# Optimization experiments

Measured on AMD Instinct MI355X. Metric: run time of the kernel, lower is better.

The kernel has to match this reference:

```python
import jax, jax.numpy as jnp
import numpy as np

B, NQ, NK, D, H = 2, 2048, 4096, 1024, 16
HD = D // H
SCALE = HD ** -0.5
NEG = -1e20


def setup_inputs() -> dict:
    key = jax.random.key(0)
    ks = jax.random.split(key, 9)
    w_std = D ** -0.5
    return {
        "q": jax.random.normal(ks[0], (B, NQ, D), dtype=jnp.float32),
        "k": jax.random.normal(ks[1], (B, NK, D), dtype=jnp.float32),
        "v": jax.random.normal(ks[2], (B, NK, D), dtype=jnp.float32),
        "key_padding_mask": jax.random.bernoulli(ks[3], 0.1, (B, NK)),
        "Wq": jax.random.normal(ks[4], (D, D), dtype=jnp.float32) * w_std,
        "Wk": jax.random.normal(ks[5], (D, D), dtype=jnp.float32) * w_std,
        "Wv": jax.random.normal(ks[6], (D, D), dtype=jnp.float32) * w_std,
        "Wp": jax.random.normal(ks[7], (D, D), dtype=jnp.float32) * w_std,
        "bp": jax.random.normal(ks[8], (D,), dtype=jnp.float32) * 0.01,
    }


def reference(q, k, v, key_padding_mask, Wq, Wk, Wv, Wp, bp):
    # linear projections (no bias, qkv_bias=False)
    qh = (q @ Wq.T).reshape(B, NQ, H, HD).transpose(0, 2, 1, 3)  # [B,H,NQ,HD]
    kh = (k @ Wk.T).reshape(B, NK, H, HD).transpose(0, 2, 1, 3)  # [B,H,NK,HD]
    vh = (v @ Wv.T).reshape(B, NK, H, HD).transpose(0, 2, 1, 3)  # [B,H,NK,HD]
    scores = jnp.einsum("bhqd,bhkd->bhqk", qh, kh)               # [B,H,NQ,NK]
    # mask BEFORE scaling (faithful to original order), then scale + softmax
    scores = jnp.where(key_padding_mask[:, None, None, :], NEG, scores)
    attn = jax.nn.softmax(scores * SCALE, axis=-1)
    out = jnp.einsum("bhqk,bhkd->bhqd", attn, vh)                # [B,H,NQ,HD]
    out = out.transpose(0, 2, 1, 3).reshape(B, NQ, D)
    x = out @ Wp.T + bp
    return x
```

## Files before the change

### kernel.cpp

```cpp
#include <hip/hip_runtime.h>


typedef __attribute__((ext_vector_type(8))) short bf16x8;
typedef __attribute__((ext_vector_type(4))) short bf16x4;
typedef __attribute__((ext_vector_type(4))) float f32x4;
typedef __attribute__((ext_vector_type(4))) unsigned short u16x4;
typedef unsigned short u16;
typedef unsigned char u8;

#define DEV __device__ __forceinline__

DEV u16 f2bf(float f) {
  union { float f; unsigned int u; } x; x.f = f;
  unsigned int u = x.u;
  return (u16)((u + 0x7fffu + ((u >> 16) & 1u)) >> 16);
}

DEV unsigned cvt_pk_bf16(float lo, float hi) {
  unsigned r;
  asm("v_cvt_pk_bf16_f32 %0, %1, %2" : "=v"(r) : "v"(lo), "v"(hi));
  return r;
}

DEV u16x4 cvt4_bf16(float4 v) {
  union { unsigned u[2]; u16x4 s; } uu;
  uu.u[0] = cvt_pk_bf16(v.x, v.y);
  uu.u[1] = cvt_pk_bf16(v.z, v.w);
  return uu.s;
}

DEV void gload16(const void* g, void* l) {
  __builtin_amdgcn_global_load_lds(
      (const __attribute__((address_space(1))) void*)g,
      (__attribute__((address_space(3))) void*)l, 16, 0, 0);
}

#define MASK_BIAS (-1.8033688e19f)
#define FREE_BIAS (-16.0f)
#define SCALE_LOG2E 0.18033688f

__global__ void prep_k(
    const float* __restrict__ Wq, const float* __restrict__ Wk,
    const float* __restrict__ Wv, const float* __restrict__ Wp,
    const float* __restrict__ q, const float* __restrict__ k, const float* __restrict__ v,
    u16* __restrict__ wqb, u16* __restrict__ wkb, u16* __restrict__ wvb, u16* __restrict__ wpb,
    u16* __restrict__ qb, u16* __restrict__ kb, u16* __restrict__ vb, int total,
    const u8* __restrict__ raw, float* __restrict__ biasf)
{
  if (blockIdx.x == gridDim.x - 1) {
    int t = threadIdx.x;
    int f_off = 0, f_gt1 = 0, f_80 = 0;
    for (int i = t; i < 8192; i += 256) {
      u8 bv = raw[i];
      if (bv > 1) f_gt1 = 1;
      if ((i & 3) && bv) f_off = 1;
      if (((i & 3) == 0) && bv == 0x80) f_80 = 1;
    }
    int g_gt1 = __syncthreads_or(f_gt1);
    int g_off = __syncthreads_or(f_off);
    int g_80  = __syncthreads_or(f_80);
    for (int i = t; i < 8192; i += 256) {
      int vv;
      if (g_gt1) {
        if (g_80) vv = (((const u16*)raw)[i] != 0) ? 1 : 0;
        else      vv = (((const float*)raw)[i] != 0.0f) ? 1 : 0;
      } else if (g_off) {
        vv = raw[i] ? 1 : 0;
      } else {
        vv = (((const int*)raw)[i] != 0) ? 1 : 0;
      }
      biasf[i] = vv ? MASK_BIAS : FREE_BIAS;
    }
    return;
  }
  int stride = (gridDim.x - 1) * blockDim.x;
  for (int idx = blockIdx.x * blockDim.x + threadIdx.x; idx < total; idx += stride) {
    const float* src; u16* dst; int off;
    if (idx < 131072)       { src = Wq; dst = wqb; off = idx; }
    else if (idx < 262144)  { src = Wk; dst = wkb; off = idx - 131072; }
    else if (idx < 393216)  { src = Wv; dst = wvb; off = idx - 262144; }
    else if (idx < 524288)  { src = Wp; dst = wpb; off = idx - 393216; }
    else if (idx < 1048576) { src = q;  dst = qb;  off = idx - 524288; }
    else if (idx < 2097152) { src = k;  dst = kb;  off = idx - 1048576; }
    else                    { src = v;  dst = vb;  off = idx - 2097152; }
    float4 a = *reinterpret_cast<const float4*>(src + (size_t)off * 8);
    float4 bq = *reinterpret_cast<const float4*>(src + (size_t)off * 8 + 4);
    union { unsigned u[4]; uint4 q4; } o;
    o.u[0] = cvt_pk_bf16(a.x, a.y); o.u[1] = cvt_pk_bf16(a.z, a.w);
    o.u[2] = cvt_pk_bf16(bq.x, bq.y); o.u[3] = cvt_pk_bf16(bq.z, bq.w);
    *reinterpret_cast<uint4*>(dst + (size_t)off * 8) = o.q4;
  }
}

template <bool ABF>
__global__ __launch_bounds__(256) void proj_fused(
    const float* __restrict__ qf32, const float* __restrict__ kf32, const float* __restrict__ vf32,
    const u16* __restrict__ qb, const u16* __restrict__ kb, const u16* __restrict__ vb,
    const u16* __restrict__ wqb, const u16* __restrict__ wkb, const u16* __restrict__ wvb,
    u16* __restrict__ qh, u16* __restrict__ kh, u16* __restrict__ vh)
{
  constexpr int K = 1024;
  __shared__ __align__(16) u16 As[128 * 32];
  __shared__ __align__(16) u16 Bs[128 * 32];
  const int tid = threadIdx.x;
  const int lane = tid & 63;
  const int w = tid >> 6;
  const int wm = w >> 1, wn = w & 1;
  const int l15 = lane & 15, lg = lane >> 4;

  int bid = blockIdx.x;
  bid = (bid & 7) * 160 + (bid >> 3);
  int seg, local;
  if (bid < 256)      { seg = 0; local = bid; }
  else if (bid < 768) { seg = 1; local = bid - 256; }
  else                { seg = 2; local = bid - 768; }
  const int bm = local >> 3, bn = local & 7;
  const float* Af = seg == 0 ? qf32 : (seg == 1 ? kf32 : vf32);
  const u16* Ab   = seg == 0 ? qb   : (seg == 1 ? kb   : vb);
  const u16* Wb   = seg == 0 ? wqb  : (seg == 1 ? wkb  : wvb);
  u16* outh       = seg == 0 ? qh   : (seg == 1 ? kh   : vh);
  const int sl = (seg == 0) ? 11 : 12;

  f32x4 acc[4][4] = {};

  for (int k0 = 0; k0 < K; k0 += 32) {
    __syncthreads();
    if constexpr (ABF) {
#pragma unroll
      for (int i = 0; i < 2; ++i) {
        int f = tid + 256 * i;
        int row = f >> 2, c = f & 3;
        gload16(Ab + (size_t)(bm * 128 + row) * K + k0 + c * 8, (char*)As + f * 16);
        gload16(Wb + (size_t)(bn * 128 + row) * K + k0 + c * 8, (char*)Bs + f * 16);
      }
    } else {
#pragma unroll
      for (int i = 0; i < 2; ++i) {
        int f = tid + 256 * i;
        int row = f >> 2, c = f & 3;
        gload16(Wb + (size_t)(bn * 128 + row) * K + k0 + c * 8, (char*)Bs + f * 16);
      }
#pragma unroll
      for (int i = 0; i < 4; ++i) {
        int f = tid + 256 * i;
        int row = f >> 3, c4 = f & 7;
        float4 va = *reinterpret_cast<const float4*>(Af + (size_t)(bm * 128 + row) * K + k0 + c4 * 4);
        *reinterpret_cast<u16x4*>((char*)As + row * 64 + c4 * 8) = cvt4_bf16(va);
      }
    }
    __syncthreads();

    bf16x8 af[4], bfr[4];
#pragma unroll
    for (int mi = 0; mi < 4; ++mi)
      af[mi] = *reinterpret_cast<const bf16x8*>((const char*)As + (wm * 64 + mi * 16 + l15) * 64 + lg * 16);
#pragma unroll
    for (int ni = 0; ni < 4; ++ni)
      bfr[ni] = *reinterpret_cast<const bf16x8*>((const char*)Bs + (wn * 64 + ni * 16 + l15) * 64 + lg * 16);
#pragma unroll
    for (int mi = 0; mi < 4; ++mi)
#pragma unroll
      for (int ni = 0; ni < 4; ++ni)
        acc[mi][ni] = __builtin_amdgcn_mfma_f32_16x16x32_bf16(af[mi], bfr[ni], acc[mi][ni], 0, 0, 0);
  }

  const int seqmask = (1 << sl) - 1;
#pragma unroll
  for (int mi = 0; mi < 4; ++mi)
#pragma unroll
    for (int ni = 0; ni < 4; ++ni)
#pragma unroll
      for (int r = 0; r < 4; ++r) {
        int m = bm * 128 + wm * 64 + mi * 16 + lg * 4 + r;
        int n = bn * 128 + wn * 64 + ni * 16 + l15;
        int b = m >> sl, ml = m & seqmask;
        int h = n >> 6, hd = n & 63;
        outh[((((size_t)b * 16 + h) << sl) + ml) * 64 + hd] = f2bf(acc[mi][ni][r]);
      }
}

__global__ __launch_bounds__(512, 2) void attn_k(
    const u16* __restrict__ qh, const u16* __restrict__ kh, const u16* __restrict__ vh,
    const float* __restrict__ biasf, u16* __restrict__ ao)
{
  __shared__ __align__(16) u16 lds[17920];

  const int tid = threadIdx.x;
  const int lane = tid & 63;
  const int w = tid >> 6;
  const int l15 = lane & 15, lg = lane >> 4;

  int bid = blockIdx.x;
  bid = (bid & 7) * 32 + (bid >> 3);
  const int qt = bid & 7;
  const int bh = bid >> 3;
  const int b = bh >> 4, h = bh & 15;

  const size_t base_kv = (size_t)bh * 4096 * 64;

  bf16x8 qf0[2], qf1[2];
  {
    const u16* qp0 = qh + ((size_t)bh * 2048 + (size_t)qt * 256 + w * 16 + l15) * 64 + lg * 8;
    qf0[0] = *reinterpret_cast<const bf16x8*>(qp0);
    qf0[1] = *reinterpret_cast<const bf16x8*>(qp0 + 32);
    const u16* qp1 = qp0 + 128 * 64;
    qf1[0] = *reinterpret_cast<const bf16x8*>(qp1);
    qf1[1] = *reinterpret_cast<const bf16x8*>(qp1 + 32);
  }

  f32x4 o0[4] = {}, o1[4] = {};
  float lac0 = 0.f, lac1 = 0.f;
  const float* bpt = biasf + b * 4096 + lg * 4;

  const int kp = tid >> 3, c8v = tid & 7;
  const u16* kg = kh + base_kv + (size_t)tid * 8;
  const u16* vg = vh + base_kv + (size_t)(2 * kp) * 64 + c8v * 8;
  const int kcol = (tid & 7) * 8;
  const int krow0 = tid >> 3, krow1 = krow0 + 32;
  int vst[8];
#pragma unroll
  for (int j = 0; j < 8; ++j) {
    int d = c8v * 8 + j;
    vst[j] = (d * 136 + kp * 4) ^ (((d >> 3) & 7) << 3);
  }
  int vrd[4][4];
#pragma unroll
  for (int dt = 0; dt < 4; ++dt)
#pragma unroll
    for (int n = 0; n < 4; ++n) {
      int d = dt * 16 + l15;
      vrd[dt][n] = ((d * 136 + (n * 16 + lg * 4) * 2)) ^ (((d >> 3) & 7) << 3);
    }

  uint4 kr0, kr1, vr0, vr1;
  if (w < 4) {
    kr0 = *reinterpret_cast<const uint4*>(kg);
    kr1 = *reinterpret_cast<const uint4*>(kg + 2048);
    vr0 = *reinterpret_cast<const uint4*>(vg);
    vr1 = *reinterpret_cast<const uint4*>(vg + 64);
    u16 (*K0)[72] = reinterpret_cast<u16(*)[72]>(lds);
    u16* V0 = lds + 4608;
    *reinterpret_cast<uint4*>(&K0[krow0][kcol]) = kr0;
    *reinterpret_cast<uint4*>(&K0[krow1][kcol]) = kr1;
    const u16* pa = reinterpret_cast<const u16*>(&vr0);
    const u16* pb = reinterpret_cast<const u16*>(&vr1);
#pragma unroll
    for (int j = 0; j < 8; ++j) {
      ushort2 t2; t2.x = pa[j]; t2.y = pb[j];
      *reinterpret_cast<ushort2*>(reinterpret_cast<char*>(V0) + vst[j]) = t2;
    }
    kg += 4096; vg += 4096;
    kr0 = *reinterpret_cast<const uint4*>(kg);
    kr1 = *reinterpret_cast<const uint4*>(kg + 2048);
    vr0 = *reinterpret_cast<const uint4*>(vg);
    vr1 = *reinterpret_cast<const uint4*>(vg + 64);
  }
  __syncthreads();

  for (int t = 0; t < 64; ++t) {
    u16* bufc = lds + (t & 1) * 8960;
    u16 (*Ks)[72] = reinterpret_cast<u16(*)[72]>(bufc);
    u16* Vt = bufc + 4608;

    if (w < 4 && t < 63) {
      u16* bufn = lds + ((t & 1) ^ 1) * 8960;
      u16 (*Kn)[72] = reinterpret_cast<u16(*)[72]>(bufn);
      u16* Vn = bufn + 4608;
      *reinterpret_cast<uint4*>(&Kn[krow0][kcol]) = kr0;
      *reinterpret_cast<uint4*>(&Kn[krow1][kcol]) = kr1;
      const u16* pa = reinterpret_cast<const u16*>(&vr0);
      const u16* pb = reinterpret_cast<const u16*>(&vr1);
#pragma unroll
      for (int j = 0; j < 8; ++j) {
        ushort2 t2; t2.x = pa[j]; t2.y = pb[j];
        *reinterpret_cast<ushort2*>(reinterpret_cast<char*>(Vn) + vst[j]) = t2;
      }
      if (t < 62) {
        kg += 4096; vg += 4096;
        kr0 = *reinterpret_cast<const uint4*>(kg);
        kr1 = *reinterpret_cast<const uint4*>(kg + 2048);
        vr0 = *reinterpret_cast<const uint4*>(vg);
        vr1 = *reinterpret_cast<const uint4*>(vg + 64);
      }
    }

    float4 bA[4];
#pragma unroll
    for (int n = 0; n < 4; ++n)
      bA[n] = *reinterpret_cast<const float4*>(bpt + n * 16);

    f32x4 s0[4], s1[4];
    __builtin_amdgcn_s_setprio(1);
#pragma unroll
    for (int n = 0; n < 4; ++n) {
      bf16x8 k0f = *reinterpret_cast<const bf16x8*>(&Ks[n * 16 + l15][lg * 8]);
      bf16x8 k1f = *reinterpret_cast<const bf16x8*>(&Ks[n * 16 + l15][32 + lg * 8]);
      f32x4 z0 = {};
      z0 = __builtin_amdgcn_mfma_f32_16x16x32_bf16(k0f, qf0[0], z0, 0, 0, 0);
      z0 = __builtin_amdgcn_mfma_f32_16x16x32_bf16(k1f, qf0[1], z0, 0, 0, 0);
      s0[n] = z0;
      f32x4 z1 = {};
      z1 = __builtin_amdgcn_mfma_f32_16x16x32_bf16(k0f, qf1[0], z1, 0, 0, 0);
      z1 = __builtin_amdgcn_mfma_f32_16x16x32_bf16(k1f, qf1[1], z1, 0, 0, 0);
      s1[n] = z1;
    }
    __builtin_amdgcn_s_setprio(0);

    bf16x4 pbf0[4], pbf1[4];
#pragma unroll
    for (int n = 0; n < 4; ++n) {
      float p0 = __builtin_amdgcn_exp2f(fmaf(s0[n][0], SCALE_LOG2E, bA[n].x));
      float p1 = __builtin_amdgcn_exp2f(fmaf(s0[n][1], SCALE_LOG2E, bA[n].y));
      float p2 = __builtin_amdgcn_exp2f(fmaf(s0[n][2], SCALE_LOG2E, bA[n].z));
      float p3 = __builtin_amdgcn_exp2f(fmaf(s0[n][3], SCALE_LOG2E, bA[n].w));
      lac0 += (p0 + p1) + (p2 + p3);
      union { unsigned u[2]; bf16x4 v; } uu;
      uu.u[0] = cvt_pk_bf16(p0, p1);
      uu.u[1] = cvt_pk_bf16(p2, p3);
      pbf0[n] = uu.v;
    }
#pragma unroll
    for (int n = 0; n < 4; ++n) {
      float p0 = __builtin_amdgcn_exp2f(fmaf(s1[n][0], SCALE_LOG2E, bA[n].x));
      float p1 = __builtin_amdgcn_exp2f(fmaf(s1[n][1], SCALE_LOG2E, bA[n].y));
      float p2 = __builtin_amdgcn_exp2f(fmaf(s1[n][2], SCALE_LOG2E, bA[n].z));
      float p3 = __builtin_amdgcn_exp2f(fmaf(s1[n][3], SCALE_LOG2E, bA[n].w));
      lac1 += (p0 + p1) + (p2 + p3);
      union { unsigned u[2]; bf16x4 v; } uu;
      uu.u[0] = cvt_pk_bf16(p0, p1);
      uu.u[1] = cvt_pk_bf16(p2, p3);
      pbf1[n] = uu.v;
    }

    __builtin_amdgcn_s_setprio(1);
#pragma unroll
    for (int dt = 0; dt < 4; ++dt)
#pragma unroll
      for (int n = 0; n < 4; ++n) {
        bf16x4 va = *reinterpret_cast<const bf16x4*>(
            reinterpret_cast<char*>(Vt) + vrd[dt][n]);
        o0[dt] = __builtin_amdgcn_mfma_f32_16x16x16bf16_1k(va, pbf0[n], o0[dt], 0, 0, 0);
        o1[dt] = __builtin_amdgcn_mfma_f32_16x16x16bf16_1k(va, pbf1[n], o1[dt], 0, 0, 0);
      }
    __builtin_amdgcn_s_setprio(0);

    bpt += 64;
    __syncthreads();
  }

  float lr0 = lac0;
  lr0 += __shfl_xor(lr0, 16, 64);
  lr0 += __shfl_xor(lr0, 32, 64);
  float lr1 = lac1;
  lr1 += __shfl_xor(lr1, 16, 64);
  lr1 += __shfl_xor(lr1, 32, 64);
  float rl0 = __builtin_amdgcn_rcpf(fmaxf(lr0, 1e-30f));
  float rl1 = __builtin_amdgcn_rcpf(fmaxf(lr1, 1e-30f));

  u16 (*Es)[64] = reinterpret_cast<u16(*)[64]>(lds);
#pragma unroll
  for (int dt = 0; dt < 4; ++dt) {
    unsigned a0 = cvt_pk_bf16(o0[dt][0] * rl0, o0[dt][1] * rl0);
    unsigned a1 = cvt_pk_bf16(o0[dt][2] * rl0, o0[dt][3] * rl0);
    *reinterpret_cast<unsigned*>(&Es[w * 16 + l15][dt * 16 + lg * 4]) = a0;
    *reinterpret_cast<unsigned*>(&Es[w * 16 + l15][dt * 16 + lg * 4 + 2]) = a1;
    unsigned b0 = cvt_pk_bf16(o1[dt][0] * rl1, o1[dt][1] * rl1);
    unsigned b1 = cvt_pk_bf16(o1[dt][2] * rl1, o1[dt][3] * rl1);
    *reinterpret_cast<unsigned*>(&Es[128 + w * 16 + l15][dt * 16 + lg * 4]) = b0;
    *reinterpret_cast<unsigned*>(&Es[128 + w * 16 + l15][dt * 16 + lg * 4 + 2]) = b1;
  }
  asm volatile("s_waitcnt lgkmcnt(0)" ::: "memory");
#pragma unroll
  for (int g = 0; g < 2; ++g) {
    int qr = lane >> 2, dc = (lane & 3) * 16;
    int lr = g * 128 + w * 16 + qr;
    uint4 x0 = *reinterpret_cast<const uint4*>(&Es[lr][dc]);
    uint4 x1 = *reinterpret_cast<const uint4*>(&Es[lr][dc + 8]);
    u16* dst = ao + ((size_t)b * 2048 + (size_t)qt * 256 + lr) * 1024 + h * 64 + dc;
    *reinterpret_cast<uint4*>(dst) = x0;
    *reinterpret_cast<uint4*>(dst + 8) = x1;
  }
}

__global__ __launch_bounds__(256) void out_gemm(
    const u16* __restrict__ Abf, const u16* __restrict__ Wb,
    const float* __restrict__ bias, float* __restrict__ out)
{
  constexpr int K = 1024, N = 1024;
  __shared__ __align__(16) u16 As[128 * 32];
  __shared__ __align__(16) u16 Bs[128 * 32];
  const int tid = threadIdx.x;
  const int lane = tid & 63;
  const int w = tid >> 6;
  const int wm = w >> 1, wn = w & 1;
  const int bm = blockIdx.x, bn = blockIdx.y;
  const int l15 = lane & 15, lg = lane >> 4;

  f32x4 acc[4][4] = {};

  for (int k0 = 0; k0 < K; k0 += 32) {
    __syncthreads();
#pragma unroll
    for (int i = 0; i < 2; ++i) {
      int f = tid + 256 * i;
      int row = f >> 2, c = f & 3;
      gload16(Abf + (size_t)(bm * 128 + row) * K + k0 + c * 8, (char*)As + f * 16);
      gload16(Wb + (size_t)(bn * 128 + row) * K + k0 + c * 8, (char*)Bs + f * 16);
    }
    __syncthreads();

    bf16x8 af[4], bfr[4];
#pragma unroll
    for (int mi = 0; mi < 4; ++mi)
      af[mi] = *reinterpret_cast<const bf16x8*>((const char*)As + (wm * 64 + mi * 16 + l15) * 64 + lg * 16);
#pragma unroll
    for (int ni = 0; ni < 4; ++ni)
      bfr[ni] = *reinterpret_cast<const bf16x8*>((const char*)Bs + (wn * 64 + ni * 16 + l15) * 64 + lg * 16);
#pragma unroll
    for (int mi = 0; mi < 4; ++mi)
#pragma unroll
      for (int ni = 0; ni < 4; ++ni)
        acc[mi][ni] = __builtin_amdgcn_mfma_f32_16x16x32_bf16(af[mi], bfr[ni], acc[mi][ni], 0, 0, 0);
  }

#pragma unroll
  for (int mi = 0; mi < 4; ++mi)
#pragma unroll
    for (int ni = 0; ni < 4; ++ni)
#pragma unroll
      for (int r = 0; r < 4; ++r) {
        int m = bm * 128 + wm * 64 + mi * 16 + lg * 4 + r;
        int n = bn * 128 + wn * 64 + ni * 16 + l15;
        out[(size_t)m * N + n] = acc[mi][ni][r] + bias[n];
      }
}

extern "C" void kernel_launch(void* const* d_in, const int* in_sizes, int n_in,
                              void* d_out, int out_size, void* d_ws, size_t ws_size,
                              hipStream_t stream) {
  const float* q  = (const float*)d_in[0];
  const float* k  = (const float*)d_in[1];
  const float* v  = (const float*)d_in[2];
  const u8* mask_raw = (const u8*)d_in[3];
  const float* Wq = (const float*)d_in[4];
  const float* Wk = (const float*)d_in[5];
  const float* Wv = (const float*)d_in[6];
  const float* Wp = (const float*)d_in[7];
  const float* bp = (const float*)d_in[8];
  float* out = (float*)d_out;

  char* ws = (char*)d_ws;
  u16* qh = (u16*)(ws);
  u16* kh = (u16*)(ws + 8388608);
  u16* vh = (u16*)(ws + 25165824);
  u16* ao = (u16*)(ws + 41943040);
  float* biasf = (float*)(ws + 50331648);
  u16* wqb = (u16*)(ws + 50364416);
  u16* wkb = (u16*)(ws + 52461568);
  u16* wvb = (u16*)(ws + 54558720);
  u16* wpb = (u16*)(ws + 56655872);
  u16* qb  = (u16*)(ws + 58753024);
  u16* kb  = (u16*)(ws + 67141632);
  u16* vb  = (u16*)(ws + 83918848);
  const size_t need_full = 100696064;

  const bool full = ws_size >= need_full;
  prep_k<<<2049, 256, 0, stream>>>(Wq, Wk, Wv, Wp, q, k, v,
                                   wqb, wkb, wvb, wpb, qb, kb, vb,
                                   full ? 3145728 : 524288, mask_raw, biasf);
  if (full) {
    proj_fused<true><<<1280, 256, 0, stream>>>(q, k, v, qb, kb, vb,
                                               wqb, wkb, wvb, qh, kh, vh);
  } else {
    proj_fused<false><<<1280, 256, 0, stream>>>(q, k, v, qb, kb, vb,
                                                wqb, wkb, wvb, qh, kh, vh);
  }
  attn_k<<<256, 512, 0, stream>>>(qh, kh, vh, biasf, ao);
  out_gemm<<<dim3(32, 8), 256, 0, stream>>>(ao, wpb, bp, out);
}
```

Measured before the change: 210.5 us.

## Switch attention QK and PV to 32x32x16 MFMA tiles with swizzled K layout

Rewrites the attention inner loop to use 32x32x16 bf16 MFMA instructions for both QK^T and PV instead of 16x16 variants. Each wave now owns 32 query rows, the K tile uses an XOR-swizzled LDS layout to avoid bank conflicts, and P fragments are rearranged across half-waves with shuffles. The aim is fewer MFMA issues and LDS reads per tile and cheaper row-sum reductions. The cost is extra cross-lane shuffles and different register pressure, and the epilogue now needs a block barrier before the staged output is read back.

```diff
diff --git a/kernel.cpp b/kernel.cpp
--- a/kernel.cpp
+++ b/kernel.cpp
@@ -4,6 +4,7 @@
 typedef __attribute__((ext_vector_type(8))) short bf16x8;
 typedef __attribute__((ext_vector_type(4))) short bf16x4;
 typedef __attribute__((ext_vector_type(4))) float f32x4;
+typedef __attribute__((ext_vector_type(16))) float f32x16;
 typedef __attribute__((ext_vector_type(4))) unsigned short u16x4;
 typedef unsigned short u16;
 typedef unsigned char u8;
@@ -179,6 +180,40 @@
       }
 }
 
+#define SM_G2(ZV, PPV, KOFF, G2) do {                                          \
+    float4 bv_ = *reinterpret_cast<const float4*>(bpt + (KOFF) + (G2) * 8);    \
+    float q0_ = __builtin_amdgcn_exp2f(fmaf(ZV[(G2)*4+0], SCALE_LOG2E, bv_.x));\
+    float q1_ = __builtin_amdgcn_exp2f(fmaf(ZV[(G2)*4+1], SCALE_LOG2E, bv_.y));\
+    float q2_ = __builtin_amdgcn_exp2f(fmaf(ZV[(G2)*4+2], SCALE_LOG2E, bv_.z));\
+    float q3_ = __builtin_amdgcn_exp2f(fmaf(ZV[(G2)*4+3], SCALE_LOG2E, bv_.w));\
+    lac += (q0_ + q1_) + (q2_ + q3_);                                          \
+    PPV[(G2)*4+0] = q0_; PPV[(G2)*4+1] = q1_;                                  \
+    PPV[(G2)*4+2] = q2_; PPV[(G2)*4+3] = q3_;                                  \
+  } while (0)
+
+#define PV_KC(PPV, KC) do {                                                    \
+    unsigned X0_ = cvt_pk_bf16(PPV[((KC)&1)*8+0], PPV[((KC)&1)*8+1]);          \
+    unsigned X1_ = cvt_pk_bf16(PPV[((KC)&1)*8+2], PPV[((KC)&1)*8+3]);          \
+    unsigned Y0_ = cvt_pk_bf16(PPV[((KC)&1)*8+4], PPV[((KC)&1)*8+5]);          \
+    unsigned Y1_ = cvt_pk_bf16(PPV[((KC)&1)*8+6], PPV[((KC)&1)*8+7]);          \
+    unsigned sX0_ = (unsigned)__shfl_xor((int)X0_, 32, 64);                    \
+    unsigned sX1_ = (unsigned)__shfl_xor((int)X1_, 32, 64);                    \
+    unsigned sY0_ = (unsigned)__shfl_xor((int)Y0_, 32, 64);                    \
+    unsigned sY1_ = (unsigned)__shfl_xor((int)Y1_, 32, 64);                    \
+    union { unsigned u[4]; bf16x8 v; } pf_;                                    \
+    pf_.u[0] = hi ? sY0_ : X0_;                                                \
+    pf_.u[1] = hi ? sY1_ : X1_;                                                \
+    pf_.u[2] = hi ? Y0_ : sX0_;                                                \
+    pf_.u[3] = hi ? Y1_ : sX1_;                                                \
+    union { u16x4 h[2]; bf16x8 v; } v0_, v1_;                                  \
+    v0_.h[0] = *reinterpret_cast<const u16x4*>(Vb + vrd[0][KC][0]);            \
+    v0_.h[1] = *reinterpret_cast<const u16x4*>(Vb + vrd[0][KC][1]);            \
+    v1_.h[0] = *reinterpret_cast<const u16x4*>(Vb + vrd[1][KC][0]);            \
+    v1_.h[1] = *reinterpret_cast<const u16x4*>(Vb + vrd[1][KC][1]);            \
+    oa0 = __builtin_amdgcn_mfma_f32_32x32x16_bf16(v0_.v, pf_.v, oa0, 0, 0, 0); \
+    oa1 = __builtin_amdgcn_mfma_f32_32x32x16_bf16(v1_.v, pf_.v, oa1, 0, 0, 0); \
+  } while (0)
+
 __global__ __launch_bounds__(512, 2) void attn_k(
     const u16* __restrict__ qh, const u16* __restrict__ kh, const u16* __restrict__ vh,
     const float* __restrict__ biasf, u16* __restrict__ ao)
@@ -188,7 +223,7 @@
   const int tid = threadIdx.x;
   const int lane = tid & 63;
   const int w = tid >> 6;
-  const int l15 = lane & 15, lg = lane >> 4;
+  const int l31 = lane & 31, hi = lane >> 5;
 
   int bid = blockIdx.x;
   bid = (bid & 7) * 32 + (bid >> 3);
@@ -198,38 +233,48 @@
 
   const size_t base_kv = (size_t)bh * 4096 * 64;
 
-  bf16x8 qf0[2], qf1[2];
+  bf16x8 qf[4];
   {
-    const u16* qp0 = qh + ((size_t)bh * 2048 + (size_t)qt * 256 + w * 16 + l15) * 64 + lg * 8;
-    qf0[0] = *reinterpret_cast<const bf16x8*>(qp0);
-    qf0[1] = *reinterpret_cast<const bf16x8*>(qp0 + 32);
-    const u16* qp1 = qp0 + 128 * 64;
-    qf1[0] = *reinterpret_cast<const bf16x8*>(qp1);
-    qf1[1] = *reinterpret_cast<const bf16x8*>(qp1 + 32);
-  }
-
-  f32x4 o0[4] = {}, o1[4] = {};
-  float lac0 = 0.f, lac1 = 0.f;
-  const float* bpt = biasf + b * 4096 + lg * 4;
+    const u16* qp = qh + ((size_t)bh * 2048 + (size_t)qt * 256 + w * 32 + l31) * 64 + hi * 8;
+    qf[0] = *reinterpret_cast<const bf16x8*>(qp);
+    qf[1] = *reinterpret_cast<const bf16x8*>(qp + 16);
+    qf[2] = *reinterpret_cast<const bf16x8*>(qp + 32);
+    qf[3] = *reinterpret_cast<const bf16x8*>(qp + 48);
+  }
+
+  f32x16 oa0 = {}, oa1 = {};
+  float lac = 0.f;
+  const float* bpt = biasf + b * 4096 + hi * 4;
 
   const int kp = tid >> 3, c8v = tid & 7;
   const u16* kg = kh + base_kv + (size_t)tid * 8;
   const u16* vg = vh + base_kv + (size_t)(2 * kp) * 64 + c8v * 8;
-  const int kcol = (tid & 7) * 8;
-  const int krow0 = tid >> 3, krow1 = krow0 + 32;
+  const int kst0 = (tid >> 3) * 144 + (((tid & 7) ^ ((tid >> 6) & 3)) << 4);
+  const int kst1 = kst0 + 4608;
   int vst[8];
 #pragma unroll
   for (int j = 0; j < 8; ++j) {
     int d = c8v * 8 + j;
     vst[j] = (d * 136 + kp * 4) ^ (((d >> 3) & 7) << 3);
   }
-  int vrd[4][4];
-#pragma unroll
-  for (int dt = 0; dt < 4; ++dt)
-#pragma unroll
-    for (int n = 0; n < 4; ++n) {
-      int d = dt * 16 + l15;
-      vrd[dt][n] = ((d * 136 + (n * 16 + lg * 4) * 2)) ^ (((d >> 3) & 7) << 3);
+
+  const int xk = (l31 >> 3) & 3;
+  int krd[2][4];
+#pragma unroll
+  for (int kt = 0; kt < 2; ++kt)
+#pragma unroll
+    for (int d16 = 0; d16 < 4; ++d16)
+      krd[kt][d16] = (kt * 32 + l31) * 144 + (((d16 * 2 + hi) ^ xk) << 4);
+  int vrd[2][4][2];
+#pragma unroll
+  for (int dt = 0; dt < 2; ++dt)
+#pragma unroll
+    for (int kc = 0; kc < 4; ++kc) {
+      int d = dt * 32 + l31;
+      int X = ((d >> 3) & 7) << 3;
+      int bb = d * 136 + kc * 32 + hi * 16;
+      vrd[dt][kc][0] = bb ^ X;
+      vrd[dt][kc][1] = (bb + 8) ^ X;
     }
 
   uint4 kr0, kr1, vr0, vr1;
@@ -238,16 +283,16 @@
     kr1 = *reinterpret_cast<const uint4*>(kg + 2048);
     vr0 = *reinterpret_cast<const uint4*>(vg);
     vr1 = *reinterpret_cast<const uint4*>(vg + 64);
-    u16 (*K0)[72] = reinterpret_cast<u16(*)[72]>(lds);
-    u16* V0 = lds + 4608;
-    *reinterpret_cast<uint4*>(&K0[krow0][kcol]) = kr0;
-    *reinterpret_cast<uint4*>(&K0[krow1][kcol]) = kr1;
+    char* Kb = (char*)lds;
+    char* Vb0 = (char*)lds + 9216;
+    *reinterpret_cast<uint4*>(Kb + kst0) = kr0;
+    *reinterpret_cast<uint4*>(Kb + kst1) = kr1;
     const u16* pa = reinterpret_cast<const u16*>(&vr0);
     const u16* pb = reinterpret_cast<const u16*>(&vr1);
 #pragma unroll
     for (int j = 0; j < 8; ++j) {
       ushort2 t2; t2.x = pa[j]; t2.y = pb[j];
-      *reinterpret_cast<ushort2*>(reinterpret_cast<char*>(V0) + vst[j]) = t2;
+      *reinterpret_cast<ushort2*>(Vb0 + vst[j]) = t2;
     }
     kg += 4096; vg += 4096;
     kr0 = *reinterpret_cast<const uint4*>(kg);
@@ -258,22 +303,20 @@
   __syncthreads();
 
   for (int t = 0; t < 64; ++t) {
-    u16* bufc = lds + (t & 1) * 8960;
-    u16 (*Ks)[72] = reinterpret_cast<u16(*)[72]>(bufc);
-    u16* Vt = bufc + 4608;
+    char* basec = (char*)(lds + (t & 1) * 8960);
+    char* Kb = basec;
+    char* Vb = basec + 9216;
 
     if (w < 4 && t < 63) {
-      u16* bufn = lds + ((t & 1) ^ 1) * 8960;
-      u16 (*Kn)[72] = reinterpret_cast<u16(*)[72]>(bufn);
-      u16* Vn = bufn + 4608;
-      *reinterpret_cast<uint4*>(&Kn[krow0][kcol]) = kr0;
-      *reinterpret_cast<uint4*>(&Kn[krow1][kcol]) = kr1;
+      char* basen = (char*)(lds + ((t & 1) ^ 1) * 8960);
+      *reinterpret_cast<uint4*>(basen + kst0) = kr0;
+      *reinterpret_cast<uint4*>(basen + kst1) = kr1;
       const u16* pa = reinterpret_cast<const u16*>(&vr0);
       const u16* pb = reinterpret_cast<const u16*>(&vr1);
 #pragma unroll
       for (int j = 0; j < 8; ++j) {
         ushort2 t2; t2.x = pa[j]; t2.y = pb[j];
-        *reinterpret_cast<ushort2*>(reinterpret_cast<char*>(Vn) + vst[j]) = t2;
+        *reinterpret_cast<ushort2*>(basen + 9216 + vst[j]) = t2;
       }
       if (t < 62) {
         kg += 4096; vg += 4096;
@@ -284,101 +327,62 @@
       }
     }
 
-    float4 bA[4];
-#pragma unroll
-    for (int n = 0; n < 4; ++n)
-      bA[n] = *reinterpret_cast<const float4*>(bpt + n * 16);
-
-    f32x4 s0[4], s1[4];
+    f32x16 z0 = {}, z1 = {};
     __builtin_amdgcn_s_setprio(1);
 #pragma unroll
-    for (int n = 0; n < 4; ++n) {
-      bf16x8 k0f = *reinterpret_cast<const bf16x8*>(&Ks[n * 16 + l15][lg * 8]);
-      bf16x8 k1f = *reinterpret_cast<const bf16x8*>(&Ks[n * 16 + l15][32 + lg * 8]);
-      f32x4 z0 = {};
-      z0 = __builtin_amdgcn_mfma_f32_16x16x32_bf16(k0f, qf0[0], z0, 0, 0, 0);
-      z0 = __builtin_amdgcn_mfma_f32_16x16x32_bf16(k1f, qf0[1], z0, 0, 0, 0);
-      s0[n] = z0;
-      f32x4 z1 = {};
-      z1 = __builtin_amdgcn_mfma_f32_16x16x32_bf16(k0f, qf1[0], z1, 0, 0, 0);
-      z1 = __builtin_amdgcn_mfma_f32_16x16x32_bf16(k1f, qf1[1], z1, 0, 0, 0);
-      s1[n] = z1;
+    for (int d16 = 0; d16 < 4; ++d16) {
+      bf16x8 k0 = *reinterpret_cast<const bf16x8*>(Kb + krd[0][d16]);
+      bf16x8 k1 = *reinterpret_cast<const bf16x8*>(Kb + krd[1][d16]);
+      z0 = __builtin_amdgcn_mfma_f32_32x32x16_bf16(k0, qf[d16], z0, 0, 0, 0);
+      z1 = __builtin_amdgcn_mfma_f32_32x32x16_bf16(k1, qf[d16], z1, 0, 0, 0);
     }
     __builtin_amdgcn_s_setprio(0);
 
-    bf16x4 pbf0[4], pbf1[4];
-#pragma unroll
-    for (int n = 0; n < 4; ++n) {
-      float p0 = __builtin_amdgcn_exp2f(fmaf(s0[n][0], SCALE_LOG2E, bA[n].x));
-      float p1 = __builtin_amdgcn_exp2f(fmaf(s0[n][1], SCALE_LOG2E, bA[n].y));
-      float p2 = __builtin_amdgcn_exp2f(fmaf(s0[n][2], SCALE_LOG2E, bA[n].z));
-      float p3 = __builtin_amdgcn_exp2f(fmaf(s0[n][3], SCALE_LOG2E, bA[n].w));
-      lac0 += (p0 + p1) + (p2 + p3);
-      union { unsigned u[2]; bf16x4 v; } uu;
-      uu.u[0] = cvt_pk_bf16(p0, p1);
-      uu.u[1] = cvt_pk_bf16(p2, p3);
-      pbf0[n] = uu.v;
-    }
-#pragma unroll
-    for (int n = 0; n < 4; ++n) {
-      float p0 = __builtin_amdgcn_exp2f(fmaf(s1[n][0], SCALE_LOG2E, bA[n].x));
-      float p1 = __builtin_amdgcn_exp2f(fmaf(s1[n][1], SCALE_LOG2E, bA[n].y));
-      float p2 = __builtin_amdgcn_exp2f(fmaf(s1[n][2], SCALE_LOG2E, bA[n].z));
-      float p3 = __builtin_amdgcn_exp2f(fmaf(s1[n][3], SCALE_LOG2E, bA[n].w));
-      lac1 += (p0 + p1) + (p2 + p3);
-      union { unsigned u[2]; bf16x4 v; } uu;
-      uu.u[0] = cvt_pk_bf16(p0, p1);
-      uu.u[1] = cvt_pk_bf16(p2, p3);
-      pbf1[n] = uu.v;
-    }
+    f32x16 p0v, p1v;
+    SM_G2(z0, p0v, 0, 0); SM_G2(z0, p0v, 0, 1);
+    SM_G2(z0, p0v, 0, 2); SM_G2(z0, p0v, 0, 3);
+    SM_G2(z1, p1v, 32, 0); SM_G2(z1, p1v, 32, 1);
+    SM_G2(z1, p1v, 32, 2); SM_G2(z1, p1v, 32, 3);
 
     __builtin_amdgcn_s_setprio(1);
-#pragma unroll
-    for (int dt = 0; dt < 4; ++dt)
-#pragma unroll
-      for (int n = 0; n < 4; ++n) {
-        bf16x4 va = *reinterpret_cast<const bf16x4*>(
-            reinterpret_cast<char*>(Vt) + vrd[dt][n]);
-        o0[dt] = __builtin_amdgcn_mfma_f32_16x16x16bf16_1k(va, pbf0[n], o0[dt], 0, 0, 0);
-        o1[dt] = __builtin_amdgcn_mfma_f32_16x16x16bf16_1k(va, pbf1[n], o1[dt], 0, 0, 0);
-      }
+    PV_KC(p0v, 0); PV_KC(p0v, 1);
+    PV_KC(p1v, 2); PV_KC(p1v, 3);
     __builtin_amdgcn_s_setprio(0);
 
     bpt += 64;
     __syncthreads();
   }
 
-  float lr0 = lac0;
-  lr0 += __shfl_xor(lr0, 16, 64);
-  lr0 += __shfl_xor(lr0, 32, 64);
-  float lr1 = lac1;
-  lr1 += __shfl_xor(lr1, 16, 64);
-  lr1 += __shfl_xor(lr1, 32, 64);
-  float rl0 = __builtin_amdgcn_rcpf(fmaxf(lr0, 1e-30f));
-  float rl1 = __builtin_amdgcn_rcpf(fmaxf(lr1, 1e-30f));
-
-  u16 (*Es)[64] = reinterpret_cast<u16(*)[64]>(lds);
-#pragma unroll
-  for (int dt = 0; dt < 4; ++dt) {
-    unsigned a0 = cvt_pk_bf16(o0[dt][0] * rl0, o0[dt][1] * rl0);
-    unsigned a1 = cvt_pk_bf16(o0[dt][2] * rl0, o0[dt][3] * rl0);
-    *reinterpret_cast<unsigned*>(&Es[w * 16 + l15][dt * 16 + lg * 4]) = a0;
-    *reinterpret_cast<unsigned*>(&Es[w * 16 + l15][dt * 16 + lg * 4 + 2]) = a1;
-    unsigned b0 = cvt_pk_bf16(o1[dt][0] * rl1, o1[dt][1] * rl1);
-    unsigned b1 = cvt_pk_bf16(o1[dt][2] * rl1, o1[dt][3] * rl1);
-    *reinterpret_cast<unsigned*>(&Es[128 + w * 16 + l15][dt * 16 + lg * 4]) = b0;
-    *reinterpret_cast<unsigned*>(&Es[128 + w * 16 + l15][dt * 16 + lg * 4 + 2]) = b1;
-  }
-  asm volatile("s_waitcnt lgkmcnt(0)" ::: "memory");
+  float lrow = lac + __shfl_xor(lac, 32, 64);
+  float rl = __builtin_amdgcn_rcpf(fmaxf(lrow, 1e-30f));
+
+  u16 (*Es)[68] = reinterpret_cast<u16(*)[68]>(lds);
+  const int qlocal = w * 32 + l31;
+#pragma unroll
+  for (int g2 = 0; g2 < 4; ++g2) {
+    int d0 = 8 * g2 + 4 * hi;
+    unsigned a0 = cvt_pk_bf16(oa0[4 * g2 + 0] * rl, oa0[4 * g2 + 1] * rl);
+    unsigned a1 = cvt_pk_bf16(oa0[4 * g2 + 2] * rl, oa0[4 * g2 + 3] * rl);
+    *reinterpret_cast<unsigned*>(&Es[qlocal][d0]) = a0;
+    *reinterpret_cast<unsigned*>(&Es[qlocal][d0 + 2]) = a1;
+    unsigned b0 = cvt_pk_bf16(oa1[4 * g2 + 0] * rl, oa1[4 * g2 + 1] * rl);
+    unsigned b1 = cvt_pk_bf16(oa1[4 * g2 + 2] * rl, oa1[4 * g2 + 3] * rl);
+    *reinterpret_cast<unsigned*>(&Es[qlocal][32 + d0]) = b0;
+    *reinterpret_cast<unsigned*>(&Es[qlocal][32 + d0 + 2]) = b1;
+  }
+  __syncthreads();
 #pragma unroll
   for (int g = 0; g < 2; ++g) {
     int qr = lane >> 2, dc = (lane & 3) * 16;
     int lr = g * 128 + w * 16 + qr;
-    uint4 x0 = *reinterpret_cast<const uint4*>(&Es[lr][dc]);
-    uint4 x1 = *reinterpret_cast<const uint4*>(&Es[lr][dc + 8]);
+    union { u16x4 h[4]; uint4 q4[2]; } xx;
+    xx.h[0] = *reinterpret_cast<const u16x4*>(&Es[lr][dc]);
+    xx.h[1] = *reinterpret_cast<const u16x4*>(&Es[lr][dc + 4]);
+    xx.h[2] = *reinterpret_cast<const u16x4*>(&Es[lr][dc + 8]);
+    xx.h[3] = *reinterpret_cast<const u16x4*>(&Es[lr][dc + 12]);
     u16* dst = ao + ((size_t)b * 2048 + (size_t)qt * 256 + lr) * 1024 + h * 64 + dc;
-    *reinterpret_cast<uint4*>(dst) = x0;
-    *reinterpret_cast<uint4*>(dst + 8) = x1;
+    *reinterpret_cast<uint4*>(dst) = xx.q4[0];
+    *reinterpret_cast<uint4*>(dst + 8) = xx.q4[1];
   }
 }
 
```

Measured after the change: 237.7 us. 1.13x slower.
